# Performance work log

Measured on AMD Instinct MI355X. Metric: run time of the kernel, lower is better.

## Reference

```python
import jax, jax.numpy as jnp
import numpy as np

T, B, F, H, W, NH = 128, 256, 128, 512, 16, 8
DK = H // NH
EPS = 1e-5  # torch BatchNorm1d default eps


def _bn(x, g, b):
    # BatchNorm1d training-mode forward: normalize over batch dim with biased var
    m = x.mean(0)
    v = x.var(0)
    return (x - m) * jax.lax.rsqrt(v + EPS) * g + b


def setup_inputs() -> dict:
    key = jax.random.key(0)
    ks = jax.random.split(key, 20)
    s = 1.0 / np.sqrt(H)  # pytorch_default init: uniform(-1/sqrt(H), 1/sqrt(H))
    u = lambda k, shp: jax.random.uniform(k, shp, jnp.float32, -s, s)
    return dict(
        x=jax.random.normal(ks[0], (T, B, F), jnp.float32),
        W_ih=u(ks[1], (F, 4 * H)), b_ih=u(ks[2], (4 * H,)),          # input_to_hidden
        W_hh=u(ks[3], (H, 4 * H)),                                    # hidden_to_hidden (no bias)
        Wq_in=u(ks[4], (F + H, H)), bq_in=u(ks[5], (H,)),             # input_and_hidden_to_query
        Wq=u(ks[6], (H, H)), bq=u(ks[7], (H,)),                       # MHA query proj
        Wk=u(ks[8], (H, H)), bk=u(ks[9], (H,)),                       # MHA key proj
        Wv=u(ks[10], (H, H)), bv=u(ks[11], (H,)),                     # MHA value proj
        Wo=u(ks[12], (H, H)), bo=u(ks[13], (H,)),                     # MHA output proj
        W_ac=u(ks[14], (H, 4 * H)), b_ac=u(ks[15], (4 * H,)),         # attention_to_cell (residual mode)
        g_att=jnp.ones((H,), jnp.float32), be_att=jnp.zeros((H,), jnp.float32),
        g_post=jnp.ones((H,), jnp.float32), be_post=jnp.zeros((H,), jnp.float32),
    )


def reference(x, W_ih, b_ih, W_hh, Wq_in, bq_in, Wq, bq, Wk, bk, Wv, bv, Wo, bo,
              W_ac, b_ac, g_att, be_att, g_post, be_post):
    scale = 1.0 / np.sqrt(DK)

    def step(carry, x_t):
        buf, mask, h, c = carry  # buf: [W,B,H] past cells, mask: [W] valid slots
        # Q = elu(Linear(cat[x, h]))
        ih = jnp.concatenate([x_t, h], -1)                      # [B,F+H]
        q = jax.nn.elu(ih @ Wq_in + bq_in)                      # [B,H]
        # Multi-head attention over past-cell window (K = V = past cells)
        Qh = (q @ Wq + bq).reshape(B, NH, DK)                   # [B,NH,DK]
        K = jax.nn.elu(buf @ Wk + bk).reshape(W, B, NH, DK)     # activation_on_keys_and_values
        V = jax.nn.elu(buf @ Wv + bv).reshape(W, B, NH, DK)
        scores = jnp.einsum('bhd,wbhd->bhw', Qh, K) * scale     # [B,NH,W]
        scores = jnp.where(mask[None, None, :], scores, -1e30)
        attn = jax.nn.softmax(scores, -1)
        ctx = jnp.einsum('bhw,wbhd->bhd', attn, V).reshape(B, H)
        att = _bn(jax.nn.elu(ctx @ Wo + bo), g_att, be_att)     # elu then batch_norm_attention_result
        # residual mode: Wx*x + Wh*h + Wa*a + b (pre-activation BN in source is dead code)
        pre = x_t @ W_ih + b_ih + h @ W_hh + att @ W_ac + b_ac  # [B,4H]
        iv = jnp.tanh(pre[:, :H])
        gates = jax.nn.sigmoid(pre[:, H:])
        f_g, i_g, o_g = gates[:, :H], gates[:, H:2 * H], gates[:, 2 * H:]
        c_new = iv * i_g + c * f_g
        h_new = _bn(o_g * jax.nn.elu(c_new), g_post, be_post)
        # append new cell to window (drop oldest)
        buf = jnp.concatenate([buf[1:], c_new[None]], 0)
        mask = jnp.concatenate([mask[1:], jnp.ones((1,), bool)], 0)
        return (buf, mask, h_new, c_new), h_new

    buf0 = jnp.zeros((W, B, H), x.dtype)
    mask0 = jnp.arange(W) == (W - 1)  # deque starts with one zero (h,c) state
    h0 = jnp.zeros((B, H), x.dtype)
    _, hs = jax.lax.scan(step, (buf0, mask0, h0, h0), x)
    return hs  # [T,B,H]
```

## Files before the change

kernel.cpp:

```cpp
#include <hip/hip_runtime.h>
#include <math.h>


#define T_  128
#define B_  256
#define F_  128
#define H_  512
#define W_  16
#define H4_ 2048
#define EPS_ 1e-5f
#define BH_ (B_*H_)
#define NBLK 512
#define NTHR 512
#define FSTRIDE 32

typedef __attribute__((ext_vector_type(4))) float f4;
typedef __attribute__((ext_vector_type(2))) float f2;
typedef unsigned long long u64;

__device__ __forceinline__ float eluf(float x){ return x > 0.f ? x : expf(x) - 1.f; }
__device__ __forceinline__ float sigf(float x){ return 1.f / (1.f + expf(-x)); }

__device__ __forceinline__ f4 ld_c(const float* p) {
  union { f4 v; u64 q[2]; } u;
  u.q[0] = __hip_atomic_load((const u64*)p,     __ATOMIC_RELAXED, __HIP_MEMORY_SCOPE_AGENT);
  u.q[1] = __hip_atomic_load((const u64*)p + 1, __ATOMIC_RELAXED, __HIP_MEMORY_SCOPE_AGENT);
  return u.v;
}
__device__ __forceinline__ void st_c(float* p, f4 v) {
  union { f4 v; u64 q[2]; } u; u.v = v;
  __hip_atomic_store((u64*)p,     u.q[0], __ATOMIC_RELAXED, __HIP_MEMORY_SCOPE_AGENT);
  __hip_atomic_store((u64*)p + 1, u.q[1], __ATOMIC_RELAXED, __HIP_MEMORY_SCOPE_AGENT);
}
__device__ __forceinline__ f2 ld2_c(const float* p) {
  union { u64 q; f2 v; } u;
  u.q = __hip_atomic_load((const u64*)p, __ATOMIC_RELAXED, __HIP_MEMORY_SCOPE_AGENT);
  return u.v;
}
__device__ __forceinline__ void st2_c(float* p, f2 v) {
  union { f2 v; u64 q; } u; u.v = v;
  __hip_atomic_store((u64*)p, u.q, __ATOMIC_RELAXED, __HIP_MEMORY_SCOPE_AGENT);
}
__device__ __forceinline__ float ldf_c(const float* p) {
  unsigned u = __hip_atomic_load((const unsigned*)p, __ATOMIC_RELAXED, __HIP_MEMORY_SCOPE_AGENT);
  return __uint_as_float(u);
}
__device__ __forceinline__ void stf_c(float* p, float v) {
  __hip_atomic_store((unsigned*)p, __float_as_uint(v), __ATOMIC_RELAXED, __HIP_MEMORY_SCOPE_AGENT);
}

struct Params {
  const float *x, *W_ih, *b_ih, *W_hh, *Wq_in, *bq_in, *Wq, *bq, *Wk, *bk,
              *Wv, *bv, *Wo, *bo, *W_ac, *b_ac, *g_att, *be_att, *g_post, *be_post;
  float *out, *c, *q, *Qh, *ctx, *attp, *hv, *pre, *Kbuf, *Vbuf, *stA, *stP;
  unsigned *gen, *arr;
};

__device__ __forceinline__ void gbar(unsigned* arr, unsigned* gen, unsigned g) {
  asm volatile("s_waitcnt vmcnt(0) lgkmcnt(0)" ::: "memory");
  __syncthreads();
  const int tid = threadIdx.x;
  if (tid == 0)
    __hip_atomic_store(&arr[blockIdx.x * FSTRIDE], g, __ATOMIC_RELAXED, __HIP_MEMORY_SCOPE_AGENT);
  if (blockIdx.x == 0) {
    if (tid < NBLK) {
      while (__hip_atomic_load(&arr[tid * FSTRIDE], __ATOMIC_RELAXED, __HIP_MEMORY_SCOPE_AGENT) < g)
        __builtin_amdgcn_s_sleep(1);
    }
    __syncthreads();
    if (tid == 0)
      __hip_atomic_store(gen, g, __ATOMIC_RELAXED, __HIP_MEMORY_SCOPE_AGENT);
  } else {
    if (tid == 0) {
      while (__hip_atomic_load(gen, __ATOMIC_RELAXED, __HIP_MEMORY_SCOPE_AGENT) < g)
        __builtin_amdgcn_s_sleep(1);
    }
  }
  __syncthreads();
}

__device__ __forceinline__ void prepP(const float* stP, const float* gn, const float* be,
                                      float* scl, float* shf, int tid) {
  if (tid < H_) {
    float S  = ldf_c(stP + tid);
    float S2 = ldf_c(stP + H_ + tid);
    float mu  = S * (1.f / B_);
    float var = S2 * (1.f / B_) - mu * mu;
    float sc  = rsqrtf(var + EPS_) * gn[tid];
    scl[tid] = sc; shf[tid] = be[tid] - mu * sc;
  }
}

__device__ __forceinline__ void prepA(const float* stA, const float* gn, const float* be,
                                      float* scl, float* shf, int tid) {
  if (tid < H_) {
    float S  = ldf_c(stA + tid) + ldf_c(stA + 1024 + tid) + ldf_c(stA + 2048 + tid) + ldf_c(stA + 3072 + tid);
    float S2 = ldf_c(stA + 512 + tid) + ldf_c(stA + 1536 + tid) + ldf_c(stA + 2560 + tid) + ldf_c(stA + 3584 + tid);
    float mu  = S * (1.f / B_);
    float var = S2 * (1.f / B_) - mu * mu;
    float sc  = rsqrtf(var + EPS_) * gn[tid];
    scl[tid] = sc; shf[tid] = be[tid] - mu * sc;
  }
}

struct GJ {
  const float* A1; int lda1; int K1; int nrm1; int cg1;
  const float* A2; int lda2; int K2; int nrm2; int cg2;
  const float* W1; const float* W2;
  const float* b1; const float* b2; const float* addm;
  float* out; float* stats;
  int N; int m0; int n0; int doElu;
};

__device__ void gemm_tile(const GJ& J, int tid,
                          float (*As)[64][36], float (*Bs)[32][36],
                          const float* scl, const float* shf) {
  const int arow = tid >> 3, akq = (tid & 7) * 4;
  const int bkk = tid >> 4, bnn = (tid & 15) * 2;
  const int ty = tid >> 4, tx = tid & 15;

  float acc[2][2] = {{0.f,0.f},{0.f,0.f}};

  f2 am0 = {0.f,0.f}, am1 = {0.f,0.f};
  if (J.addm) {
    am0 = ld2_c(J.addm + (size_t)(J.m0 + ty * 2)     * J.N + J.n0 + tx * 2);
    am1 = ld2_c(J.addm + (size_t)(J.m0 + ty * 2 + 1) * J.N + J.n0 + tx * 2);
  }

  int buf = 0;
  for (int s = 0; s < 2; ++s) {
    const float* A = s ? J.A2 : J.A1;
    if (!A) break;
    const float* Wp  = s ? J.W2 : J.W1;
    const int K      = s ? J.K2 : J.K1;
    const int lda    = s ? J.lda2 : J.lda1;
    const int nrm    = s ? J.nrm2 : J.nrm1;
    const int cg     = s ? J.cg2 : J.cg1;
    const int nsl    = K >> 5;

    const float* aBase = A + (size_t)(J.m0 + arow) * lda + akq;
    const float* wBase = Wp + (size_t)bkk * J.N + J.n0 + bnn;
    const size_t wSlab = (size_t)32 * J.N;

    f4 aN1 = cg ? ld_c(aBase) : *(const f4*)aBase;
    f4 aN2 = (nsl > 1) ? (cg ? ld_c(aBase + 32) : *(const f4*)(aBase + 32)) : aN1;
    f2 bN1 = *(const f2*)wBase;

    for (int sl = 0; sl < nsl; ++sl) {
      f4 aCur = aN1; aN1 = aN2;
      f2 bCur = bN1;
      if (sl + 2 < nsl) {
        const float* ap = aBase + (size_t)(sl + 2) * 32;
        aN2 = cg ? ld_c(ap) : *(const f4*)ap;
      }
      if (sl + 1 < nsl) bN1 = *(const f2*)(wBase + (size_t)(sl + 1) * wSlab);
      if (nrm) {
        #pragma unroll
        for (int i = 0; i < 4; ++i) {
          int gk = sl * 32 + akq + i;
          aCur[i] = aCur[i] * scl[gk] + shf[gk];
        }
      }
      *(f4*)&As[buf][arow][akq] = aCur;
      *(f2*)&Bs[buf][bkk][bnn] = bCur;
      __syncthreads();
      #pragma unroll
      for (int k = 0; k < 32; k += 2) {
        f2 a0 = *(const f2*)&As[buf][ty * 2][k];
        f2 a1 = *(const f2*)&As[buf][ty * 2 + 1][k];
        f2 b0 = *(const f2*)&Bs[buf][k][tx * 2];
        f2 b1 = *(const f2*)&Bs[buf][k + 1][tx * 2];
        acc[0][0] = fmaf(a0[0], b0[0], acc[0][0]);
        acc[0][1] = fmaf(a0[0], b0[1], acc[0][1]);
        acc[0][0] = fmaf(a0[1], b1[0], acc[0][0]);
        acc[0][1] = fmaf(a0[1], b1[1], acc[0][1]);
        acc[1][0] = fmaf(a1[0], b0[0], acc[1][0]);
        acc[1][1] = fmaf(a1[0], b0[1], acc[1][1]);
        acc[1][0] = fmaf(a1[1], b1[0], acc[1][0]);
        acc[1][1] = fmaf(a1[1], b1[1], acc[1][1]);
      }
      buf ^= 1;
    }
  }

  const int r0 = J.m0 + ty * 2, c0 = J.n0 + tx * 2;
  f2 bias = {0.f, 0.f};
  if (J.b1) bias += *(const f2*)(J.b1 + c0);
  if (J.b2) bias += *(const f2*)(J.b2 + c0);
  f2 v0, v1;
  v0[0] = acc[0][0] + bias[0]; v0[1] = acc[0][1] + bias[1];
  v1[0] = acc[1][0] + bias[0]; v1[1] = acc[1][1] + bias[1];
  if (J.addm) { v0 += am0; v1 += am1; }
  if (J.doElu) {
    v0[0] = eluf(v0[0]); v0[1] = eluf(v0[1]);
    v1[0] = eluf(v1[0]); v1[1] = eluf(v1[1]);
  }
  st2_c(J.out + (size_t)r0 * J.N + c0, v0);
  st2_c(J.out + (size_t)(r0 + 1) * J.N + c0, v1);

  if (J.stats) {
    float* Af = (float*)As;
    float* Bf = (float*)Bs;
    __syncthreads();
    Af[ty * 32 + tx * 2]     = v0[0] + v1[0];
    Af[ty * 32 + tx * 2 + 1] = v0[1] + v1[1];
    Bf[ty * 32 + tx * 2]     = v0[0] * v0[0] + v1[0] * v1[0];
    Bf[ty * 32 + tx * 2 + 1] = v0[1] * v0[1] + v1[1] * v1[1];
    __syncthreads();
    if (tid < 32) {
      float S = 0.f, S2 = 0.f;
      #pragma unroll
      for (int y = 0; y < 32; ++y) { S += Af[y * 32 + tid]; S2 += Bf[y * 32 + tid]; }
      const int tm = J.m0 >> 6;
      stf_c(J.stats + tm * 1024 + J.n0 + tid, S);
      stf_c(J.stats + tm * 1024 + 512 + J.n0 + tid, S2);
    }
  }
}

__global__ __launch_bounds__(NTHR, 4) void larnn(Params P) {
  __shared__ float As[2][64][36];
  __shared__ float Bs[2][32][36];
  __shared__ float scl[H_], shf[H_];
  __shared__ float Qs[H_];
  __shared__ float sc_[8][16], aw_[8][16];

  const int bid = blockIdx.x, tid = threadIdx.x;
  unsigned g = 0;

  for (int t = 0; t < T_; ++t) {
    const float* xt = P.x + (size_t)t * B_ * F_;
    const int slot = (t - 1) & 15;

    if (bid < 64) {
      if (t > 0) { prepP(P.stP, P.g_post, P.be_post, scl, shf, tid); __syncthreads(); }
      GJ J = {}; J.A1 = xt; J.lda1 = F_; J.K1 = F_;
      if (t > 0) { J.A2 = P.hv; J.lda2 = H_; J.K2 = H_; J.nrm2 = 1; J.cg2 = 1; }
      J.W1 = P.Wq_in; J.W2 = P.Wq_in + (size_t)F_ * H_;
      J.b1 = P.bq_in; J.out = P.q; J.N = H_;
      J.m0 = (bid >> 4) * 64; J.n0 = (bid & 15) * 32; J.doElu = 1;
      gemm_tile(J, tid, As, Bs, scl, shf);
    } else if (bid < 128) {
      int l = bid - 64;
      GJ J = {}; J.A1 = P.c; J.lda1 = H_; J.K1 = H_; J.cg1 = 1;
      J.W1 = P.Wk; J.b1 = P.bk; J.out = P.Kbuf + (size_t)slot * BH_; J.N = H_;
      J.m0 = (l >> 4) * 64; J.n0 = (l & 15) * 32; J.doElu = 1;
      gemm_tile(J, tid, As, Bs, scl, shf);
    } else if (bid < 192) {
      int l = bid - 128;
      GJ J = {}; J.A1 = P.c; J.lda1 = H_; J.K1 = H_; J.cg1 = 1;
      J.W1 = P.Wv; J.b1 = P.bv; J.out = P.Vbuf + (size_t)slot * BH_; J.N = H_;
      J.m0 = (l >> 4) * 64; J.n0 = (l & 15) * 32; J.doElu = 1;
      gemm_tile(J, tid, As, Bs, scl, shf);
    } else if (bid < 448) {
      if (t > 0) { prepP(P.stP, P.g_post, P.be_post, scl, shf, tid); __syncthreads(); }
      const int ix = bid - 192;
      GJ J = {}; J.A1 = xt; J.lda1 = F_; J.K1 = F_;
      if (t > 0) { J.A2 = P.hv; J.lda2 = H_; J.K2 = H_; J.nrm2 = 1; J.cg2 = 1; }
      J.W1 = P.W_ih; J.W2 = P.W_hh;
      J.b1 = P.b_ih; J.b2 = P.b_ac; J.out = P.pre; J.N = H4_;
      J.m0 = (ix >> 6) * 64; J.n0 = (ix & 63) * 32;
      gemm_tile(J, tid, As, Bs, scl, shf);
    } else if (bid < 480 && t > 0) {
      prepP(P.stP, P.g_post, P.be_post, scl, shf, tid);
      __syncthreads();
      const int rb0 = (bid - 448) * 8;
      for (int idx = tid; idx < 1024; idx += NTHR) {
        int r = rb0 + (idx >> 7), cc = (idx & 127) * 4;
        f4 hvv = ld_c(P.hv + (size_t)r * H_ + cc);
        f4 v;
        #pragma unroll
        for (int i = 0; i < 4; ++i) v[i] = hvv[i] * scl[cc + i] + shf[cc + i];
        *(f4*)(P.out + (size_t)(t - 1) * BH_ + (size_t)r * H_ + cc) = v;
      }
    }
    gbar(P.arr, P.gen, ++g);

    if (bid < 64) {
      GJ J = {}; J.A1 = P.q; J.lda1 = H_; J.K1 = H_; J.cg1 = 1;
      J.W1 = P.Wq; J.b1 = P.bq; J.out = P.Qh; J.N = H_;
      J.m0 = (bid >> 4) * 64; J.n0 = (bid & 15) * 32;
      gemm_tile(J, tid, As, Bs, scl, shf);
    }
    gbar(P.arr, P.gen, ++g);

    if (bid < B_) {
      const int b = bid;
      const int nv = (t + 1 < W_) ? t + 1 : W_;
      if (tid < 128) *(f4*)&Qs[tid * 4] = ld_c(P.Qh + (size_t)b * H_ + tid * 4);
      __syncthreads();
      {
        const int p = tid >> 2, l4 = tid & 3;
        const int hh = p >> 4, w = p & 15;
        if (w < nv) {
          const int sl = (t - 1 - w) & 15;
          const float* kp = P.Kbuf + ((size_t)sl * B_ + b) * H_ + hh * 64 + l4 * 16;
          const float* qp = Qs + hh * 64 + l4 * 16;
          float s = 0.f;
          #pragma unroll
          for (int d = 0; d < 16; d += 4) {
            f4 kv = ld_c(kp + d);
            f4 qv = *(const f4*)(qp + d);
            s = fmaf(kv[0], qv[0], fmaf(kv[1], qv[1], fmaf(kv[2], qv[2], fmaf(kv[3], qv[3], s))));
          }
          s += __shfl_xor(s, 1); s += __shfl_xor(s, 2);
          if (l4 == 0) sc_[hh][w] = s * 0.125f;
        }
      }
      __syncthreads();
      if (tid < 8) {
        float mx = -1e30f;
        for (int w = 0; w < nv; ++w) mx = fmaxf(mx, sc_[tid][w]);
        float ss = 0.f;
        for (int w = 0; w < nv; ++w) { float e = expf(sc_[tid][w] - mx); aw_[tid][w] = e; ss += e; }
        float inv = 1.f / ss;
        for (int w = 0; w < nv; ++w) aw_[tid][w] *= inv;
      }
      __syncthreads();
      {
        const int j = tid, hh = j >> 6;
        float o = 0.f;
        for (int w = 0; w < nv; ++w) {
          const int sl = (t - 1 - w) & 15;
          o = fmaf(aw_[hh][w], ldf_c(P.Vbuf + ((size_t)sl * B_ + b) * H_ + j), o);
        }
        stf_c(P.ctx + (size_t)b * H_ + j, o);
      }
    }
    gbar(P.arr, P.gen, ++g);

    if (bid < 64) {
      GJ J = {}; J.A1 = P.ctx; J.lda1 = H_; J.K1 = H_; J.cg1 = 1;
      J.W1 = P.Wo; J.b1 = P.bo; J.doElu = 1;
      J.out = P.attp; J.stats = P.stA; J.N = H_;
      J.m0 = (bid >> 4) * 64; J.n0 = (bid & 15) * 32;
      gemm_tile(J, tid, As, Bs, scl, shf);
    }
    gbar(P.arr, P.gen, ++g);

    if (bid < 256) {
      prepA(P.stA, P.g_att, P.be_att, scl, shf, tid);
      __syncthreads();
      GJ J = {}; J.A1 = P.attp; J.lda1 = H_; J.K1 = H_; J.cg1 = 1; J.nrm1 = 1;
      J.W1 = P.W_ac; J.addm = P.pre; J.out = P.pre; J.N = H4_;
      J.m0 = (bid >> 6) * 64; J.n0 = (bid & 63) * 32;
      gemm_tile(J, tid, As, Bs, scl, shf);
    }
    gbar(P.arr, P.gen, ++g);

    if (bid < 64) {
      f4* rS = (f4*)As;
      f4* rQ = (f4*)Bs;
      const int sub = tid & 1, r = tid >> 1;
      const int c4 = bid * 8 + sub * 4;
      const size_t rb = (size_t)r * H4_;
      f4 p0 = ld_c(P.pre + rb + c4);
      f4 pf = ld_c(P.pre + rb + c4 + 512);
      f4 pi = ld_c(P.pre + rb + c4 + 1024);
      f4 po = ld_c(P.pre + rb + c4 + 1536);
      const size_t ci = (size_t)r * H_ + c4;
      f4 cold = ld_c(P.c + ci);
      f4 cn, hvv;
      #pragma unroll
      for (int i = 0; i < 4; ++i) {
        float iv = tanhf(p0[i]);
        float fg = sigf(pf[i]), ig = sigf(pi[i]), og = sigf(po[i]);
        cn[i] = iv * ig + cold[i] * fg;
        hvv[i] = og * eluf(cn[i]);
      }
      st_c(P.c + ci, cn);
      st_c(P.hv + ci, hvv);
      rS[sub * 256 + r] = hvv;
      rQ[sub * 256 + r] = hvv * hvv;
      __syncthreads();
      for (int s2 = 128; s2 > 0; s2 >>= 1) {
        if (r < s2) {
          rS[sub * 256 + r] += rS[sub * 256 + r + s2];
          rQ[sub * 256 + r] += rQ[sub * 256 + r + s2];
        }
        __syncthreads();
      }
      if (r == 0) {
        f4 S = rS[sub * 256], Q2 = rQ[sub * 256];
        #pragma unroll
        for (int i = 0; i < 4; ++i) { stf_c(P.stP + c4 + i, S[i]); stf_c(P.stP + 512 + c4 + i, Q2[i]); }
      }
    }
    gbar(P.arr, P.gen, ++g);
  }

  if (bid >= 448 && bid < 480) {
    prepP(P.stP, P.g_post, P.be_post, scl, shf, tid);
    __syncthreads();
    const int rb0 = (bid - 448) * 8;
    for (int idx = tid; idx < 1024; idx += NTHR) {
      int r = rb0 + (idx >> 7), cc = (idx & 127) * 4;
      f4 hvv = ld_c(P.hv + (size_t)r * H_ + cc);
      f4 v;
      #pragma unroll
      for (int i = 0; i < 4; ++i) v[i] = hvv[i] * scl[cc + i] + shf[cc + i];
      *(f4*)(P.out + (size_t)127 * BH_ + (size_t)r * H_ + cc) = v;
    }
  }
}

#define SYNC_UINTS (32 + NBLK * FSTRIDE)

__global__ __launch_bounds__(256) void pinit(float* c, unsigned* sync) {
  const int i = blockIdx.x * 256 + threadIdx.x;
  if (i < BH_) c[i] = 0.f;
  if (i < SYNC_UINTS) sync[i] = 0u;
}

extern "C" void kernel_launch(void* const* d_in, const int* in_sizes, int n_in,
                              void* d_out, int out_size, void* d_ws, size_t ws_size,
                              hipStream_t stream) {
  Params P;
  P.x      = (const float*)d_in[0];
  P.W_ih   = (const float*)d_in[1];
  P.b_ih   = (const float*)d_in[2];
  P.W_hh   = (const float*)d_in[3];
  P.Wq_in  = (const float*)d_in[4];
  P.bq_in  = (const float*)d_in[5];
  P.Wq     = (const float*)d_in[6];
  P.bq     = (const float*)d_in[7];
  P.Wk     = (const float*)d_in[8];
  P.bk     = (const float*)d_in[9];
  P.Wv     = (const float*)d_in[10];
  P.bv     = (const float*)d_in[11];
  P.Wo     = (const float*)d_in[12];
  P.bo     = (const float*)d_in[13];
  P.W_ac   = (const float*)d_in[14];
  P.b_ac   = (const float*)d_in[15];
  P.g_att  = (const float*)d_in[16];
  P.be_att = (const float*)d_in[17];
  P.g_post = (const float*)d_in[18];
  P.be_post= (const float*)d_in[19];
  P.out    = (float*)d_out;

  unsigned* sync = (unsigned*)d_ws;
  P.gen = sync;
  P.arr = sync + 32;
  float* fb = (float*)d_ws + SYNC_UINTS;
  P.c    = fb;                 fb += BH_;
  P.q    = fb;                 fb += BH_;
  P.Qh   = fb;                 fb += BH_;
  P.ctx  = fb;                 fb += BH_;
  P.attp = fb;                 fb += BH_;
  P.hv   = fb;                 fb += BH_;
  P.pre  = fb;                 fb += (size_t)B_ * H4_;
  P.Kbuf = fb;                 fb += (size_t)W_ * BH_;
  P.Vbuf = fb;                 fb += (size_t)W_ * BH_;
  P.stA  = fb;                 fb += 4096;
  P.stP  = fb;                 fb += 1024;

  pinit<<<(BH_ + 255) / 256, 256, 0, stream>>>(P.c, sync);
  larnn<<<NBLK, NTHR, 0, stream>>>(P);
}
```

Baseline: 15.84 ms.

## Fuse attention-to-cell GEMM with LSTM gate epilogue and post-BN stats

```diff
diff --git a/kernel.cpp b/kernel.cpp
--- a/kernel.cpp
+++ b/kernel.cpp
@@ -79,23 +79,11 @@
   __syncthreads();
 }
 
-__device__ __forceinline__ void prepP(const float* stP, const float* gn, const float* be,
+__device__ __forceinline__ void prep4(const float* st, const float* gn, const float* be,
                                       float* scl, float* shf, int tid) {
   if (tid < H_) {
-    float S  = ldf_c(stP + tid);
-    float S2 = ldf_c(stP + H_ + tid);
-    float mu  = S * (1.f / B_);
-    float var = S2 * (1.f / B_) - mu * mu;
-    float sc  = rsqrtf(var + EPS_) * gn[tid];
-    scl[tid] = sc; shf[tid] = be[tid] - mu * sc;
-  }
-}
-
-__device__ __forceinline__ void prepA(const float* stA, const float* gn, const float* be,
-                                      float* scl, float* shf, int tid) {
-  if (tid < H_) {
-    float S  = ldf_c(stA + tid) + ldf_c(stA + 1024 + tid) + ldf_c(stA + 2048 + tid) + ldf_c(stA + 3072 + tid);
-    float S2 = ldf_c(stA + 512 + tid) + ldf_c(stA + 1536 + tid) + ldf_c(stA + 2560 + tid) + ldf_c(stA + 3584 + tid);
+    float S  = ldf_c(st + tid) + ldf_c(st + 1024 + tid) + ldf_c(st + 2048 + tid) + ldf_c(st + 3072 + tid);
+    float S2 = ldf_c(st + 512 + tid) + ldf_c(st + 1536 + tid) + ldf_c(st + 2560 + tid) + ldf_c(st + 3584 + tid);
     float mu  = S * (1.f / B_);
     float var = S2 * (1.f / B_) - mu * mu;
     float sc  = rsqrtf(var + EPS_) * gn[tid];
@@ -113,7 +101,7 @@
 };
 
 __device__ void gemm_tile(const GJ& J, int tid,
-                          float (*As)[64][36], float (*Bs)[32][36],
+                          float (*As)[64][36], float (*Bs)[32][68],
                           const float* scl, const float* shf) {
   const int arow = tid >> 3, akq = (tid & 7) * 4;
   const int bkk = tid >> 4, bnn = (tid & 15) * 2;
@@ -218,9 +206,109 @@
   }
 }
 
+__device__ void gemm_gates(const Params& P, int tid, int bid,
+                           float (*As)[64][36], float (*Bs)[32][68],
+                           const float* scl, const float* shf) {
+  const int m0 = (bid >> 5) * 64, n0 = (bid & 31) * 16;
+  const int arow = tid >> 3, akq = (tid & 7) * 4;
+  const int kk = tid >> 4, c8 = tid & 15;
+  const int ty = tid >> 4, tx = tid & 15;
+  const int r0 = m0 + ty * 2;
+
+  float am[2][4];
+  #pragma unroll
+  for (int i = 0; i < 2; ++i)
+    #pragma unroll
+    for (int gg = 0; gg < 4; ++gg)
+      am[i][gg] = ldf_c(P.pre + (size_t)(r0 + i) * H4_ + n0 + tx + gg * 512);
+  float cold0 = ldf_c(P.c + (size_t)r0 * H_ + n0 + tx);
+  float cold1 = ldf_c(P.c + (size_t)(r0 + 1) * H_ + n0 + tx);
+
+  const float* aBase = P.attp + (size_t)(m0 + arow) * H_ + akq;
+  const float* wBase = P.W_ac + (size_t)kk * H4_ + n0 + c8;
+
+  float acc[2][4] = {};
+
+  f4 aN1 = ld_c(aBase);
+  f4 aN2 = ld_c(aBase + 32);
+  float b0N = wBase[0], b1N = wBase[512], b2N = wBase[1024], b3N = wBase[1536];
+
+  int buf = 0;
+  for (int sl = 0; sl < 16; ++sl) {
+    f4 aCur = aN1; aN1 = aN2;
+    float b0C = b0N, b1C = b1N, b2C = b2N, b3C = b3N;
+    if (sl + 2 < 16) aN2 = ld_c(aBase + (size_t)(sl + 2) * 32);
+    if (sl + 1 < 16) {
+      const float* wp = wBase + (size_t)(sl + 1) * 32 * H4_;
+      b0N = wp[0]; b1N = wp[512]; b2N = wp[1024]; b3N = wp[1536];
+    }
+    #pragma unroll
+    for (int i = 0; i < 4; ++i) {
+      int gk = sl * 32 + akq + i;
+      aCur[i] = aCur[i] * scl[gk] + shf[gk];
+    }
+    *(f4*)&As[buf][arow][akq] = aCur;
+    f4 bv = {b0C, b1C, b2C, b3C};
+    *(f4*)&Bs[buf][kk][c8 * 4] = bv;
+    __syncthreads();
+    #pragma unroll
+    for (int k = 0; k < 32; k += 2) {
+      f2 a0 = *(const f2*)&As[buf][ty * 2][k];
+      f2 a1 = *(const f2*)&As[buf][ty * 2 + 1][k];
+      f4 bv0 = *(const f4*)&Bs[buf][k][tx * 4];
+      f4 bv1 = *(const f4*)&Bs[buf][k + 1][tx * 4];
+      #pragma unroll
+      for (int gg = 0; gg < 4; ++gg) {
+        acc[0][gg] = fmaf(a0[0], bv0[gg], acc[0][gg]);
+        acc[0][gg] = fmaf(a0[1], bv1[gg], acc[0][gg]);
+        acc[1][gg] = fmaf(a1[0], bv0[gg], acc[1][gg]);
+        acc[1][gg] = fmaf(a1[1], bv1[gg], acc[1][gg]);
+      }
+    }
+    buf ^= 1;
+  }
+
+  float s = 0.f, s2 = 0.f;
+  #pragma unroll
+  for (int i = 0; i < 2; ++i) {
+    float vA = acc[i][0] + am[i][0];
+    float vF = acc[i][1] + am[i][1];
+    float vI = acc[i][2] + am[i][2];
+    float vO = acc[i][3] + am[i][3];
+    float iv = tanhf(vA);
+    float fg = sigf(vF), ig = sigf(vI), og = sigf(vO);
+    float cold = i ? cold1 : cold0;
+    float cnew = iv * ig + cold * fg;
+    const size_t ci = (size_t)(r0 + i) * H_ + n0 + tx;
+    stf_c(P.c + ci, cnew);
+    float hv = og * eluf(cnew);
+    stf_c(P.hv + ci, hv);
+    s += hv; s2 += hv * hv;
+  }
+  float* Af = (float*)As;
+  float* Bf = (float*)Bs;
+  __syncthreads();
+  Af[ty * 16 + tx] = s;
+  Bf[ty * 16 + tx] = s2;
+  __syncthreads();
+  #pragma unroll
+  for (int off = 16; off >= 1; off >>= 1) {
+    if (ty < off) {
+      Af[ty * 16 + tx] += Af[(ty + off) * 16 + tx];
+      Bf[ty * 16 + tx] += Bf[(ty + off) * 16 + tx];
+    }
+    __syncthreads();
+  }
+  if (tid < 16) {
+    const int tm = m0 >> 6;
+    stf_c(P.stP + tm * 1024 + n0 + tid, Af[tid]);
+    stf_c(P.stP + tm * 1024 + 512 + n0 + tid, Bf[tid]);
+  }
+}
+
 __global__ __launch_bounds__(NTHR, 4) void larnn(Params P) {
   __shared__ float As[2][64][36];
-  __shared__ float Bs[2][32][36];
+  __shared__ float Bs[2][32][68];
   __shared__ float scl[H_], shf[H_];
   __shared__ float Qs[H_];
   __shared__ float sc_[8][16], aw_[8][16];
@@ -233,7 +321,7 @@
     const int slot = (t - 1) & 15;
 
     if (bid < 64) {
-      if (t > 0) { prepP(P.stP, P.g_post, P.be_post, scl, shf, tid); __syncthreads(); }
+      if (t > 0) { prep4(P.stP, P.g_post, P.be_post, scl, shf, tid); __syncthreads(); }
       GJ J = {}; J.A1 = xt; J.lda1 = F_; J.K1 = F_;
       if (t > 0) { J.A2 = P.hv; J.lda2 = H_; J.K2 = H_; J.nrm2 = 1; J.cg2 = 1; }
       J.W1 = P.Wq_in; J.W2 = P.Wq_in + (size_t)F_ * H_;
@@ -253,7 +341,7 @@
       J.m0 = (l >> 4) * 64; J.n0 = (l & 15) * 32; J.doElu = 1;
       gemm_tile(J, tid, As, Bs, scl, shf);
     } else if (bid < 448) {
-      if (t > 0) { prepP(P.stP, P.g_post, P.be_post, scl, shf, tid); __syncthreads(); }
+      if (t > 0) { prep4(P.stP, P.g_post, P.be_post, scl, shf, tid); __syncthreads(); }
       const int ix = bid - 192;
       GJ J = {}; J.A1 = xt; J.lda1 = F_; J.K1 = F_;
       if (t > 0) { J.A2 = P.hv; J.lda2 = H_; J.K2 = H_; J.nrm2 = 1; J.cg2 = 1; }
@@ -262,7 +350,7 @@
       J.m0 = (ix >> 6) * 64; J.n0 = (ix & 63) * 32;
       gemm_tile(J, tid, As, Bs, scl, shf);
     } else if (bid < 480 && t > 0) {
-      prepP(P.stP, P.g_post, P.be_post, scl, shf, tid);
+      prep4(P.stP, P.g_post, P.be_post, scl, shf, tid);
       __syncthreads();
       const int rb0 = (bid - 448) * 8;
       for (int idx = tid; idx < 1024; idx += NTHR) {
@@ -338,59 +426,16 @@
     }
     gbar(P.arr, P.gen, ++g);
 
-    if (bid < 256) {
-      prepA(P.stA, P.g_att, P.be_att, scl, shf, tid);
+    if (bid < 128) {
+      prep4(P.stA, P.g_att, P.be_att, scl, shf, tid);
       __syncthreads();
-      GJ J = {}; J.A1 = P.attp; J.lda1 = H_; J.K1 = H_; J.cg1 = 1; J.nrm1 = 1;
-      J.W1 = P.W_ac; J.addm = P.pre; J.out = P.pre; J.N = H4_;
-      J.m0 = (bid >> 6) * 64; J.n0 = (bid & 63) * 32;
-      gemm_tile(J, tid, As, Bs, scl, shf);
+      gemm_gates(P, tid, bid, As, Bs, scl, shf);
     }
     gbar(P.arr, P.gen, ++g);
-
-    if (bid < 64) {
-      f4* rS = (f4*)As;
-      f4* rQ = (f4*)Bs;
-      const int sub = tid & 1, r = tid >> 1;
-      const int c4 = bid * 8 + sub * 4;
-      const size_t rb = (size_t)r * H4_;
-      f4 p0 = ld_c(P.pre + rb + c4);
-      f4 pf = ld_c(P.pre + rb + c4 + 512);
-      f4 pi = ld_c(P.pre + rb + c4 + 1024);
-      f4 po = ld_c(P.pre + rb + c4 + 1536);
-      const size_t ci = (size_t)r * H_ + c4;
-      f4 cold = ld_c(P.c + ci);
-      f4 cn, hvv;
-      #pragma unroll
-      for (int i = 0; i < 4; ++i) {
-        float iv = tanhf(p0[i]);
-        float fg = sigf(pf[i]), ig = sigf(pi[i]), og = sigf(po[i]);
-        cn[i] = iv * ig + cold[i] * fg;
-        hvv[i] = og * eluf(cn[i]);
-      }
-      st_c(P.c + ci, cn);
-      st_c(P.hv + ci, hvv);
-      rS[sub * 256 + r] = hvv;
-      rQ[sub * 256 + r] = hvv * hvv;
-      __syncthreads();
-      for (int s2 = 128; s2 > 0; s2 >>= 1) {
-        if (r < s2) {
-          rS[sub * 256 + r] += rS[sub * 256 + r + s2];
-          rQ[sub * 256 + r] += rQ[sub * 256 + r + s2];
-        }
-        __syncthreads();
-      }
-      if (r == 0) {
-        f4 S = rS[sub * 256], Q2 = rQ[sub * 256];
-        #pragma unroll
-        for (int i = 0; i < 4; ++i) { stf_c(P.stP + c4 + i, S[i]); stf_c(P.stP + 512 + c4 + i, Q2[i]); }
-      }
-    }
-    gbar(P.arr, P.gen, ++g);
   }
 
   if (bid >= 448 && bid < 480) {
-    prepP(P.stP, P.g_post, P.be_post, scl, shf, tid);
+    prep4(P.stP, P.g_post, P.be_post, scl, shf, tid);
     __syncthreads();
     const int rb0 = (bid - 448) * 8;
     for (int idx = tid; idx < 1024; idx += NTHR) {
@@ -452,7 +497,7 @@
   P.Kbuf = fb;                 fb += (size_t)W_ * BH_;
   P.Vbuf = fb;                 fb += (size_t)W_ * BH_;
   P.stA  = fb;                 fb += 4096;
-  P.stP  = fb;                 fb += 1024;
+  P.stP  = fb;                 fb += 4096;
 
   pinit<<<(BH_ + 255) / 256, 256, 0, stream>>>(P.c, sync);
   larnn<<<NBLK, NTHR, 0, stream>>>(P);
```

Measured after the change: 28.22 ms. 78.1% more time.

## Replace two grid barriers with producer-consumer flags between Qh, attention and Wo stages

Applied to the files above, without the earlier changes.

```diff
diff --git a/kernel.cpp b/kernel.cpp
--- a/kernel.cpp
+++ b/kernel.cpp
@@ -48,12 +48,18 @@
 __device__ __forceinline__ void stf_c(float* p, float v) {
   __hip_atomic_store((unsigned*)p, __float_as_uint(v), __ATOMIC_RELAXED, __HIP_MEMORY_SCOPE_AGENT);
 }
+__device__ __forceinline__ unsigned ldu_c(const unsigned* p) {
+  return __hip_atomic_load(p, __ATOMIC_RELAXED, __HIP_MEMORY_SCOPE_AGENT);
+}
+__device__ __forceinline__ void stu_c(unsigned* p, unsigned v) {
+  __hip_atomic_store(p, v, __ATOMIC_RELAXED, __HIP_MEMORY_SCOPE_AGENT);
+}
 
 struct Params {
   const float *x, *W_ih, *b_ih, *W_hh, *Wq_in, *bq_in, *Wq, *bq, *Wk, *bk,
               *Wv, *bv, *Wo, *bo, *W_ac, *b_ac, *g_att, *be_att, *g_post, *be_post;
   float *out, *c, *q, *Qh, *ctx, *attp, *hv, *pre, *Kbuf, *Vbuf, *stA, *stP;
-  unsigned *gen, *arr;
+  unsigned *gen, *arr, *qfl, *cfl;
 };
 
 __device__ __forceinline__ void gbar(unsigned* arr, unsigned* gen, unsigned g) {
@@ -77,6 +83,12 @@
     }
   }
   __syncthreads();
+}
+
+__device__ __forceinline__ void set_flag(unsigned* fl, unsigned v, int tid) {
+  asm volatile("s_waitcnt vmcnt(0) lgkmcnt(0)" ::: "memory");
+  __syncthreads();
+  if (tid == 0) stu_c(fl, v);
 }
 
 __device__ __forceinline__ void prepP(const float* stP, const float* gn, const float* be,
@@ -231,6 +243,7 @@
   for (int t = 0; t < T_; ++t) {
     const float* xt = P.x + (size_t)t * B_ * F_;
     const int slot = (t - 1) & 15;
+    const unsigned fv = (unsigned)(t + 1);
 
     if (bid < 64) {
       if (t > 0) { prepP(P.stP, P.g_post, P.be_post, scl, shf, tid); __syncthreads(); }
@@ -276,17 +289,21 @@
     }
     gbar(P.arr, P.gen, ++g);
 
-    if (bid < 64) {
+    if (bid >= 256 && bid < 320) {
+      const int l = bid - 256;
       GJ J = {}; J.A1 = P.q; J.lda1 = H_; J.K1 = H_; J.cg1 = 1;
       J.W1 = P.Wq; J.b1 = P.bq; J.out = P.Qh; J.N = H_;
-      J.m0 = (bid >> 4) * 64; J.n0 = (bid & 15) * 32;
-      gemm_tile(J, tid, As, Bs, scl, shf);
-    }
-    gbar(P.arr, P.gen, ++g);
-
-    if (bid < B_) {
+      J.m0 = (l >> 4) * 64; J.n0 = (l & 15) * 32;
+      gemm_tile(J, tid, As, Bs, scl, shf);
+      set_flag(P.qfl + l * FSTRIDE, fv, tid);
+    } else if (bid < 256) {
       const int b = bid;
       const int nv = (t + 1 < W_) ? t + 1 : W_;
+      if (tid < 16) {
+        const unsigned* fp = P.qfl + ((b >> 6) * 16 + tid) * FSTRIDE;
+        while (ldu_c(fp) < fv) __builtin_amdgcn_s_sleep(1);
+      }
+      __syncthreads();
       if (tid < 128) *(f4*)&Qs[tid * 4] = ld_c(P.Qh + (size_t)b * H_ + tid * 4);
       __syncthreads();
       {
@@ -326,14 +343,18 @@
         }
         stf_c(P.ctx + (size_t)b * H_ + j, o);
       }
-    }
-    gbar(P.arr, P.gen, ++g);
-
-    if (bid < 64) {
+      set_flag(P.cfl + b * FSTRIDE, fv, tid);
+    } else if (bid >= 320 && bid < 384) {
+      const int l = bid - 320;
+      if (tid < 64) {
+        const unsigned* fp = P.cfl + ((l >> 4) * 64 + tid) * FSTRIDE;
+        while (ldu_c(fp) < fv) __builtin_amdgcn_s_sleep(1);
+      }
+      __syncthreads();
       GJ J = {}; J.A1 = P.ctx; J.lda1 = H_; J.K1 = H_; J.cg1 = 1;
       J.W1 = P.Wo; J.b1 = P.bo; J.doElu = 1;
       J.out = P.attp; J.stats = P.stA; J.N = H_;
-      J.m0 = (bid >> 4) * 64; J.n0 = (bid & 15) * 32;
+      J.m0 = (l >> 4) * 64; J.n0 = (l & 15) * 32;
       gemm_tile(J, tid, As, Bs, scl, shf);
     }
     gbar(P.arr, P.gen, ++g);
@@ -404,7 +425,7 @@
   }
 }
 
-#define SYNC_UINTS (32 + NBLK * FSTRIDE)
+#define SYNC_UINTS (32 + NBLK * FSTRIDE + 64 * FSTRIDE + 256 * FSTRIDE)
 
 __global__ __launch_bounds__(256) void pinit(float* c, unsigned* sync) {
   const int i = blockIdx.x * 256 + threadIdx.x;
@@ -441,6 +462,8 @@
   unsigned* sync = (unsigned*)d_ws;
   P.gen = sync;
   P.arr = sync + 32;
+  P.qfl = sync + 32 + NBLK * FSTRIDE;
+  P.cfl = P.qfl + 64 * FSTRIDE;
   float* fb = (float*)d_ws + SYNC_UINTS;
   P.c    = fb;                 fb += BH_;
   P.q    = fb;                 fb += BH_;
```

Result: no change. 15.83 ms (-0.1%).

## Precompute next step's input projections in idle blocks during the Qh phase

Applied to the files above, without the earlier changes.

```diff
diff --git a/kernel.cpp b/kernel.cpp
--- a/kernel.cpp
+++ b/kernel.cpp
@@ -53,6 +53,7 @@
   const float *x, *W_ih, *b_ih, *W_hh, *Wq_in, *bq_in, *Wq, *bq, *Wk, *bk,
               *Wv, *bv, *Wo, *bo, *W_ac, *b_ac, *g_att, *be_att, *g_post, *be_post;
   float *out, *c, *q, *Qh, *ctx, *attp, *hv, *pre, *Kbuf, *Vbuf, *stA, *stP;
+  float *preX0, *preX1, *qX0, *qX1;
   unsigned *gen, *arr;
 };
 
@@ -228,16 +229,35 @@
   const int bid = blockIdx.x, tid = threadIdx.x;
   unsigned g = 0;
 
+  if (bid < 256) {
+    GJ J = {}; J.A1 = P.x; J.lda1 = F_; J.K1 = F_;
+    J.W1 = P.W_ih; J.b1 = P.b_ih; J.b2 = P.b_ac;
+    J.out = P.preX0; J.N = H4_;
+    J.m0 = (bid >> 6) * 64; J.n0 = (bid & 63) * 32;
+    gemm_tile(J, tid, As, Bs, scl, shf);
+  } else if (bid < 320) {
+    int l = bid - 256;
+    GJ J = {}; J.A1 = P.x; J.lda1 = F_; J.K1 = F_;
+    J.W1 = P.Wq_in; J.b1 = P.bq_in;
+    J.out = P.qX0; J.N = H_;
+    J.m0 = (l >> 4) * 64; J.n0 = (l & 15) * 32;
+    gemm_tile(J, tid, As, Bs, scl, shf);
+  }
+  gbar(P.arr, P.gen, ++g);
+
   for (int t = 0; t < T_; ++t) {
-    const float* xt = P.x + (size_t)t * B_ * F_;
     const int slot = (t - 1) & 15;
+    float* preX  = (t & 1) ? P.preX1 : P.preX0;
+    float* qX    = (t & 1) ? P.qX1 : P.qX0;
+    float* preXn = (t & 1) ? P.preX0 : P.preX1;
+    float* qXn   = (t & 1) ? P.qX0 : P.qX1;
 
     if (bid < 64) {
       if (t > 0) { prepP(P.stP, P.g_post, P.be_post, scl, shf, tid); __syncthreads(); }
-      GJ J = {}; J.A1 = xt; J.lda1 = F_; J.K1 = F_;
-      if (t > 0) { J.A2 = P.hv; J.lda2 = H_; J.K2 = H_; J.nrm2 = 1; J.cg2 = 1; }
-      J.W1 = P.Wq_in; J.W2 = P.Wq_in + (size_t)F_ * H_;
-      J.b1 = P.bq_in; J.out = P.q; J.N = H_;
+      GJ J = {};
+      if (t > 0) { J.A1 = P.hv; J.lda1 = H_; J.K1 = H_; J.nrm1 = 1; J.cg1 = 1;
+                   J.W1 = P.Wq_in + (size_t)F_ * H_; }
+      J.addm = qX; J.out = P.q; J.N = H_;
       J.m0 = (bid >> 4) * 64; J.n0 = (bid & 15) * 32; J.doElu = 1;
       gemm_tile(J, tid, As, Bs, scl, shf);
     } else if (bid < 128) {
@@ -255,10 +275,10 @@
     } else if (bid < 448) {
       if (t > 0) { prepP(P.stP, P.g_post, P.be_post, scl, shf, tid); __syncthreads(); }
       const int ix = bid - 192;
-      GJ J = {}; J.A1 = xt; J.lda1 = F_; J.K1 = F_;
-      if (t > 0) { J.A2 = P.hv; J.lda2 = H_; J.K2 = H_; J.nrm2 = 1; J.cg2 = 1; }
-      J.W1 = P.W_ih; J.W2 = P.W_hh;
-      J.b1 = P.b_ih; J.b2 = P.b_ac; J.out = P.pre; J.N = H4_;
+      GJ J = {};
+      if (t > 0) { J.A1 = P.hv; J.lda1 = H_; J.K1 = H_; J.nrm1 = 1; J.cg1 = 1;
+                   J.W1 = P.W_hh; }
+      J.addm = preX; J.out = P.pre; J.N = H4_;
       J.m0 = (ix >> 6) * 64; J.n0 = (ix & 63) * 32;
       gemm_tile(J, tid, As, Bs, scl, shf);
     } else if (bid < 480 && t > 0) {
@@ -280,6 +300,20 @@
       GJ J = {}; J.A1 = P.q; J.lda1 = H_; J.K1 = H_; J.cg1 = 1;
       J.W1 = P.Wq; J.b1 = P.bq; J.out = P.Qh; J.N = H_;
       J.m0 = (bid >> 4) * 64; J.n0 = (bid & 15) * 32;
+      gemm_tile(J, tid, As, Bs, scl, shf);
+    } else if (bid < 320 && t + 1 < T_) {
+      const int ix = bid - 64;
+      GJ J = {}; J.A1 = P.x + (size_t)(t + 1) * B_ * F_; J.lda1 = F_; J.K1 = F_;
+      J.W1 = P.W_ih; J.b1 = P.b_ih; J.b2 = P.b_ac;
+      J.out = preXn; J.N = H4_;
+      J.m0 = (ix >> 6) * 64; J.n0 = (ix & 63) * 32;
+      gemm_tile(J, tid, As, Bs, scl, shf);
+    } else if (bid < 384 && t + 1 < T_) {
+      const int l = bid - 320;
+      GJ J = {}; J.A1 = P.x + (size_t)(t + 1) * B_ * F_; J.lda1 = F_; J.K1 = F_;
+      J.W1 = P.Wq_in; J.b1 = P.bq_in;
+      J.out = qXn; J.N = H_;
+      J.m0 = (l >> 4) * 64; J.n0 = (l & 15) * 32;
       gemm_tile(J, tid, As, Bs, scl, shf);
     }
     gbar(P.arr, P.gen, ++g);
@@ -442,17 +476,21 @@
   P.gen = sync;
   P.arr = sync + 32;
   float* fb = (float*)d_ws + SYNC_UINTS;
-  P.c    = fb;                 fb += BH_;
-  P.q    = fb;                 fb += BH_;
-  P.Qh   = fb;                 fb += BH_;
-  P.ctx  = fb;                 fb += BH_;
-  P.attp = fb;                 fb += BH_;
-  P.hv   = fb;                 fb += BH_;
-  P.pre  = fb;                 fb += (size_t)B_ * H4_;
-  P.Kbuf = fb;                 fb += (size_t)W_ * BH_;
-  P.Vbuf = fb;                 fb += (size_t)W_ * BH_;
-  P.stA  = fb;                 fb += 4096;
-  P.stP  = fb;                 fb += 1024;
+  P.c     = fb;                fb += BH_;
+  P.q     = fb;                fb += BH_;
+  P.Qh    = fb;                fb += BH_;
+  P.ctx   = fb;                fb += BH_;
+  P.attp  = fb;                fb += BH_;
+  P.hv    = fb;                fb += BH_;
+  P.pre   = fb;                fb += (size_t)B_ * H4_;
+  P.Kbuf  = fb;                fb += (size_t)W_ * BH_;
+  P.Vbuf  = fb;                fb += (size_t)W_ * BH_;
+  P.preX0 = fb;                fb += (size_t)B_ * H4_;
+  P.preX1 = fb;                fb += (size_t)B_ * H4_;
+  P.qX0   = fb;                fb += BH_;
+  P.qX1   = fb;                fb += BH_;
+  P.stA   = fb;                fb += 4096;
+  P.stP   = fb;                fb += 1024;
 
   pinit<<<(BH_ + 255) / 256, 256, 0, stream>>>(P.c, sync);
   larnn<<<NBLK, NTHR, 0, stream>>>(P);
```

New measurement: 34.47 ms. 118% more time.
